# Kernel tuning notes

Hardware: AMD Instinct MI355X
Metric: run time of the kernel (lower is better)

## Reference

```python
import jax, jax.numpy as jnp
import numpy as np

B_COEF = 0.1          # position-offset scale 'b'
STRIDE = (1, 1)
PADDING = (1, 1)


def setup_inputs() -> dict:
    key = jax.random.key(0)
    k1, k2, k3 = jax.random.split(key, 3)
    x = jax.random.normal(k1, (16, 64, 128, 128), dtype=jnp.float32)
    kernel = jax.random.normal(k2, (128, 64, 3, 3), dtype=jnp.float32)
    bias = jax.random.normal(k3, (128,), dtype=jnp.float32)
    return {"x": x, "kernel": kernel, "bias": bias}


def _conv(inp, w):
    pads = [(PADDING[0], PADDING[0]), (PADDING[1], PADDING[1])]
    return jax.lax.conv_general_dilated(
        inp, w, window_strides=STRIDE, padding=pads,
        dimension_numbers=("NCHW", "OIHW", "NCHW"))


def reference(x, kernel, bias):
    # out[b,o,p] = sum_i x_unf[b,i,p] * (kernel_flat[o,i] + b*grid[p]) + bias[o]
    # = conv(x, kernel) + b*grid[p] * sum_i x_unf[b,i,p] + bias  (rank-1 separable)
    kh, kw = kernel.shape[2], kernel.shape[3]
    main = _conv(x, kernel)                                  # (B, O, Ho, Wo)
    H_out, W_out = main.shape[2], main.shape[3]

    # sum over in_channels and kernel window = ones-conv of channel-summed input
    ones_k = jnp.ones((1, 1, kh, kw), dtype=x.dtype)
    patch_sum = _conv(x.sum(axis=1, keepdims=True), ones_k)  # (B, 1, Ho, Wo)

    # Replicate torch meshgrid(arange(W_out), arange(H_out), indexing='ij')
    # -> flatten (W,H) row-major -> consumed as (H,W) row-major by the view.
    gx = jnp.arange(W_out)[:, None] + jnp.arange(H_out)[None, :]  # (Wo, Ho)
    grid2d = gx.reshape(-1).reshape(H_out, W_out).astype(x.dtype)  # (Ho, Wo)

    return main + B_COEF * grid2d * patch_sum + bias[None, :, None, None]
```

## Files before the change

### kernel.cpp

```cpp
#include <hip/hip_runtime.h>
#include <hip/hip_bf16.h>


typedef __attribute__((ext_vector_type(8))) short short8;
typedef __attribute__((ext_vector_type(4))) float f32x4;

#define B_COEF 0.1f
constexpr int CI = 64, CO = 128, H = 128, W = 128;
constexpr int XPAD = 72;

static __device__ inline short bf16s(float v) {
    __hip_bfloat16 b = __float2bfloat16(v);
    return *reinterpret_cast<short*>(&b);
}


__global__ __launch_bounds__(256)
void prep_x(const float* __restrict__ x, __hip_bfloat16* __restrict__ xt,
            float* __restrict__ S) {
    __shared__ float tile[64 * 132];
    __shared__ float psum[8 * 128];
    const int bx = blockIdx.x, b = blockIdx.y, tid = threadIdx.x;
    const int h = ((bx & 7) << 4) | (bx >> 3);
    const int q = tid & 31, cbase = tid >> 5;

    const float* xp = x + (((size_t)b * CI + cbase * 8) * H + h) * W + q * 4;
    f32x4 v[8];
#pragma unroll
    for (int it = 0; it < 8; ++it)
        v[it] = *(const f32x4*)(xp + (size_t)it * H * W);

    const int cw = 4 * (q ^ cbase);
    f32x4 sacc = v[0];
#pragma unroll
    for (int it = 0; it < 8; ++it) {
        *(f32x4*)&tile[(cbase * 8 + it) * 132 + cw] = v[it];
        if (it) sacc += v[it];
    }
    *(f32x4*)&psum[cbase * 128 + 4 * q] = sacc;
    __syncthreads();

    if (tid < 128) {
        float s = 0.0f;
#pragma unroll
        for (int g = 0; g < 8; ++g) s += psum[g * 128 + tid];
        S[((size_t)b * H + h) * W + tid] = s;
    }

    const int c8 = (tid & 7) * 8, wl = tid >> 3, sw = 4 * (tid & 7);
#pragma unroll
    for (int it = 0; it < 4; ++it) {
        int ww = wl + it * 32;
        short8 pk;
#pragma unroll
        for (int j = 0; j < 8; ++j)
            pk[j] = bf16s(tile[(c8 + j) * 132 + (ww ^ sw)]);
        *(short8*)(xt + (((size_t)b * H + h) * W + ww) * CI + c8) = pk;
    }
}

__global__ void prep_wq(const float* __restrict__ wgt, __hip_bfloat16* __restrict__ wq) {
    int idx = blockIdx.x * 256 + threadIdx.x;
    if (idx < 9 * CO * CI) {
        int tap = idx >> 13;
        int rem = idx & 8191;
        int oc = rem >> 6, ci = rem & 63;
        int kc = ci >> 5, j = ci & 31;
        wq[(((tap * 2 + kc) * CO + oc) << 5) + j] =
            __float2bfloat16(wgt[(oc * CI + ci) * 9 + tap]);
    }
}

__global__ __launch_bounds__(256, 2)
void conv_main(const __hip_bfloat16* __restrict__ xt,
               const __hip_bfloat16* __restrict__ wq,
               const float* __restrict__ S,
               const float* __restrict__ bias,
               float* __restrict__ out) {
    __shared__ __hip_bfloat16 xrow[4][130 * XPAD];
    __shared__ float ssum[2][132];

    const int tid = threadIdx.x, bx = blockIdx.x, b = blockIdx.y;
    const int strip = ((bx & 7) << 3) | (bx >> 3);
    const int h0 = strip * 2;
    const int lane = tid & 63, waveid = tid >> 6;
    const int lo16 = lane & 15, quad = lane >> 4;
    const int m0 = (waveid & 1) * 64, n0 = (waveid >> 1) * 64;

    const int c8 = (tid & 7) * 8, wl = tid >> 3;
#pragma unroll
    for (int r = 0; r < 4; ++r) {
        const int gh = h0 - 1 + r;
#pragma unroll
        for (int it = 0; it < 5; ++it) {
            int w = wl + it * 32;
            if (w < 130) {
                int gw = w - 1;
                short8 v = {0, 0, 0, 0, 0, 0, 0, 0};
                if (gh >= 0 && gh < H && gw >= 0 && gw < W)
                    v = *(const short8*)(xt + (((size_t)b * H + gh) * W + gw) * CI + c8);
                *(short8*)&xrow[r][w * XPAD + c8] = v;
            }
        }
    }
    if (tid < 130) {
        int gw = tid - 1;
        float s4[4] = {0.0f, 0.0f, 0.0f, 0.0f};
        if (gw >= 0 && gw < W) {
#pragma unroll
            for (int r = 0; r < 4; ++r) {
                int gh = h0 - 1 + r;
                if (gh >= 0 && gh < H) s4[r] = S[((size_t)b * H + gh) * W + gw];
            }
        }
        ssum[0][tid] = s4[0] + s4[1] + s4[2];
        ssum[1][tid] = s4[1] + s4[2] + s4[3];
    }
    __syncthreads();

    f32x4 acc[2][4][4] = {};

#pragma unroll
    for (int kh = 0; kh < 3; ++kh) {
#pragma unroll
        for (int kw = 0; kw < 3; ++kw) {
            const int tap = kh * 3 + kw;
            short8 bq[2][4];
#pragma unroll
            for (int kc = 0; kc < 2; ++kc)
#pragma unroll
                for (int ni = 0; ni < 4; ++ni)
                    bq[kc][ni] = *(const short8*)(
                        wq + (((tap * 2 + kc) * CO + n0 + ni * 16 + lo16) << 5) + quad * 8);
#pragma unroll
            for (int r = 0; r < 2; ++r) {
#pragma unroll
                for (int kc = 0; kc < 2; ++kc) {
                    short8 af[4];
#pragma unroll
                    for (int mi = 0; mi < 4; ++mi)
                        af[mi] = *(const short8*)
                            &xrow[kh + r][(m0 + mi * 16 + lo16 + kw) * XPAD + kc * 32 + quad * 8];
#pragma unroll
                    for (int mi = 0; mi < 4; ++mi)
#pragma unroll
                        for (int ni = 0; ni < 4; ++ni)
                            acc[r][mi][ni] = __builtin_amdgcn_mfma_f32_16x16x32_bf16(
                                af[mi], bq[kc][ni], acc[r][mi][ni], 0, 0, 0);
                }
            }
        }
    }

#pragma unroll
    for (int r = 0; r < 2; ++r) {
        const int h = h0 + r;
#pragma unroll
        for (int mi = 0; mi < 4; ++mi) {
            const int wbase = m0 + mi * 16 + quad * 4;
            float cs[6];
#pragma unroll
            for (int t = 0; t < 6; ++t) cs[t] = ssum[r][wbase + t];
            float ps[4], cf[4];
#pragma unroll
            for (int t = 0; t < 4; ++t) {
                ps[t] = cs[t] + cs[t + 1] + cs[t + 2];
                cf[t] = B_COEF * (float)(h + wbase + t);
            }
#pragma unroll
            for (int ni = 0; ni < 4; ++ni) {
                const int oc = n0 + ni * 16 + lo16;
                const float bv = bias[oc];
                f32x4 vv = acc[r][mi][ni];
#pragma unroll
                for (int t = 0; t < 4; ++t) vv[t] = vv[t] + cf[t] * ps[t] + bv;
                *(f32x4*)(out + (((size_t)b * CO + oc) * H + h) * W + wbase) = vv;
            }
        }
    }
}


constexpr int WPAD = 72;

__global__ void prep_w_fb(const float* __restrict__ wgt, __hip_bfloat16* __restrict__ wt) {
    int idx = blockIdx.x * 256 + threadIdx.x;
    if (idx < 9 * CO * CI) {
        int tap = idx / (CO * CI);
        int rem = idx - tap * (CO * CI);
        int oc = rem >> 6, ci = rem & 63;
        wt[idx] = __float2bfloat16(wgt[(oc * CI + ci) * 9 + tap]);
    }
}

__global__ __launch_bounds__(256, 2)
void conv_fb(const float* __restrict__ x, const __hip_bfloat16* __restrict__ wt,
             const float* __restrict__ bias, float* __restrict__ out) {
    __shared__ __hip_bfloat16 xrow[130 * XPAD];
    __shared__ __hip_bfloat16 wlds[CO * WPAD];
    __shared__ float colsum[132];

    const int tid = threadIdx.x;
    const int h = blockIdx.x, b = blockIdx.y;
    const int lane = tid & 63, waveid = tid >> 6;
    const int lo16 = lane & 15, quad = lane >> 4;
    const int m0 = (waveid & 1) * 64, n0 = (waveid >> 1) * 64;

    f32x4 acc[4][4] = {};
    if (tid < 132) colsum[tid] = 0.0f;
    const float* xb = x + (size_t)b * CI * H * W;

    const int w16 = tid & 15, cipl = (tid >> 4) & 3, rest0 = tid >> 6;

    for (int kh = 0; kh < 3; ++kh) {
        const int gh = h - 1 + kh;
        __syncthreads();
        for (int it = 0; it < 18; ++it) {
            int rest = rest0 + it * 4;
            int whi = rest % 9, ciph = rest / 9;
            int w = whi * 16 + w16;
            int ci0 = (ciph * 4 + cipl) * 2;
            int gw = w - 1;
            float x0 = 0.0f, x1 = 0.0f;
            if (w < 130 && gw >= 0 && gw < W && gh >= 0 && gh < H) {
                const float* p = xb + (size_t)ci0 * (H * W) + gh * W + gw;
                x0 = p[0];
                x1 = p[H * W];
            }
            if (w < 130) {
                __hip_bfloat162 pk;
                pk.x = __float2bfloat16(x0);
                pk.y = __float2bfloat16(x1);
                *(__hip_bfloat162*)&xrow[w * XPAD + ci0] = pk;
            }
            float cs = x0 + x1;
            cs += __shfl_xor(cs, 16);
            cs += __shfl_xor(cs, 32);
            if (quad == 0 && w < 130) atomicAdd(&colsum[w], cs);
        }
        for (int kw = 0; kw < 3; ++kw) {
            __syncthreads();
            {
                const __hip_bfloat16* wtap = wt + (kh * 3 + kw) * (CO * CI);
#pragma unroll
                for (int it = 0; it < 4; ++it) {
                    int j = tid + it * 256;
                    int oc = j >> 3, ch = (j & 7) * 8;
                    short8 v = *(const short8*)(wtap + oc * CI + ch);
                    *(short8*)&wlds[oc * WPAD + ch] = v;
                }
            }
            __syncthreads();
#pragma unroll
            for (int kc = 0; kc < 2; ++kc) {
                const int krow = kc * 32 + quad * 8;
                short8 af[4], bf[4];
#pragma unroll
                for (int mi = 0; mi < 4; ++mi)
                    af[mi] = *(const short8*)&xrow[(m0 + mi * 16 + lo16 + kw) * XPAD + krow];
#pragma unroll
                for (int ni = 0; ni < 4; ++ni)
                    bf[ni] = *(const short8*)&wlds[(n0 + ni * 16 + lo16) * WPAD + krow];
#pragma unroll
                for (int mi = 0; mi < 4; ++mi)
#pragma unroll
                    for (int ni = 0; ni < 4; ++ni)
                        acc[mi][ni] = __builtin_amdgcn_mfma_f32_16x16x32_bf16(
                            af[mi], bf[ni], acc[mi][ni], 0, 0, 0);
            }
        }
    }
    __syncthreads();
#pragma unroll
    for (int mi = 0; mi < 4; ++mi) {
        const int wbase = m0 + mi * 16 + quad * 4;
        float cs[6];
#pragma unroll
        for (int r = 0; r < 6; ++r) cs[r] = colsum[wbase + r];
        float ps[4], cf[4];
#pragma unroll
        for (int r = 0; r < 4; ++r) {
            ps[r] = cs[r] + cs[r + 1] + cs[r + 2];
            cf[r] = B_COEF * (float)(h + wbase + r);
        }
#pragma unroll
        for (int ni = 0; ni < 4; ++ni) {
            const int oc = n0 + ni * 16 + lo16;
            const float bv = bias[oc];
            f32x4 v = acc[mi][ni];
#pragma unroll
            for (int r = 0; r < 4; ++r) v[r] = v[r] + cf[r] * ps[r] + bv;
            *(f32x4*)(out + (((size_t)b * CO + oc) * H + h) * W + wbase) = v;
        }
    }
}


extern "C" void kernel_launch(void* const* d_in, const int* in_sizes, int n_in,
                              void* d_out, int out_size, void* d_ws, size_t ws_size,
                              hipStream_t stream) {
    const float* x    = (const float*)d_in[0];
    const float* wgt  = (const float*)d_in[1];
    const float* bias = (const float*)d_in[2];
    float* out = (float*)d_out;

    const size_t XT_BYTES = (size_t)16 * H * W * CI * 2;
    const size_t S_BYTES  = (size_t)16 * H * W * 4;
    const size_t WQ_BYTES = (size_t)9 * 2 * CO * 32 * 2;

    if (ws_size >= XT_BYTES + S_BYTES + WQ_BYTES) {
        __hip_bfloat16* xt = (__hip_bfloat16*)d_ws;
        float* S           = (float*)((char*)d_ws + XT_BYTES);
        __hip_bfloat16* wq = (__hip_bfloat16*)((char*)d_ws + XT_BYTES + S_BYTES);
        prep_x<<<dim3(H, 16), dim3(256), 0, stream>>>(x, xt, S);
        prep_wq<<<dim3(288), dim3(256), 0, stream>>>(wgt, wq);
        conv_main<<<dim3(H / 2, 16), dim3(256), 0, stream>>>(xt, wq, S, bias, out);
    } else {
        __hip_bfloat16* wt = (__hip_bfloat16*)d_ws;
        prep_w_fb<<<dim3(288), dim3(256), 0, stream>>>(wgt, wt);
        conv_fb<<<dim3(H, 16), dim3(256), 0, stream>>>(x, wt, bias, out);
    }
}
```

Baseline: 257.9 us.

## Shrink conv tile to one row by half-width for higher occupancy

Each conv_main block now computes one output row and half its width (64 pixels) instead of two full rows. Each wave covers all 64 pixels for 32 output channels. Accumulators drop from 32 to 8 MFMA tiles and shared memory shrinks, which lets launch bounds ask for 4 blocks per SIMD and gives a grid four times larger for better occupancy and balance. In exchange, the halo overlap per pixel is higher and weights are reloaded per block more often, so input-row reuse falls.

```diff
diff --git a/kernel.cpp b/kernel.cpp
--- a/kernel.cpp
+++ b/kernel.cpp
@@ -71,31 +71,31 @@
     }
 }
 
-__global__ __launch_bounds__(256, 2)
+__global__ __launch_bounds__(256, 4)
 void conv_main(const __hip_bfloat16* __restrict__ xt,
                const __hip_bfloat16* __restrict__ wq,
                const float* __restrict__ S,
                const float* __restrict__ bias,
                float* __restrict__ out) {
-    __shared__ __hip_bfloat16 xrow[4][130 * XPAD];
-    __shared__ float ssum[2][132];
+    __shared__ __hip_bfloat16 xrow[3][66 * XPAD];
+    __shared__ float ssum[68];
 
     const int tid = threadIdx.x, bx = blockIdx.x, b = blockIdx.y;
-    const int strip = ((bx & 7) << 3) | (bx >> 3);
-    const int h0 = strip * 2;
+    const int u = ((bx & 7) << 5) | (bx >> 3);
+    const int h = u >> 1, w0 = (u & 1) * 64;
     const int lane = tid & 63, waveid = tid >> 6;
     const int lo16 = lane & 15, quad = lane >> 4;
-    const int m0 = (waveid & 1) * 64, n0 = (waveid >> 1) * 64;
+    const int n0 = waveid * 32;
 
     const int c8 = (tid & 7) * 8, wl = tid >> 3;
 #pragma unroll
-    for (int r = 0; r < 4; ++r) {
-        const int gh = h0 - 1 + r;
-#pragma unroll
-        for (int it = 0; it < 5; ++it) {
+    for (int r = 0; r < 3; ++r) {
+        const int gh = h - 1 + r;
+#pragma unroll
+        for (int it = 0; it < 3; ++it) {
             int w = wl + it * 32;
-            if (w < 130) {
-                int gw = w - 1;
+            if (w < 66) {
+                int gw = w0 + w - 1;
                 short8 v = {0, 0, 0, 0, 0, 0, 0, 0};
                 if (gh >= 0 && gh < H && gw >= 0 && gw < W)
                     v = *(const short8*)(xt + (((size_t)b * H + gh) * W + gw) * CI + c8);
@@ -103,79 +103,71 @@
             }
         }
     }
-    if (tid < 130) {
-        int gw = tid - 1;
-        float s4[4] = {0.0f, 0.0f, 0.0f, 0.0f};
+    if (tid < 66) {
+        int gw = w0 + tid - 1;
+        float s = 0.0f;
         if (gw >= 0 && gw < W) {
 #pragma unroll
-            for (int r = 0; r < 4; ++r) {
-                int gh = h0 - 1 + r;
-                if (gh >= 0 && gh < H) s4[r] = S[((size_t)b * H + gh) * W + gw];
-            }
-        }
-        ssum[0][tid] = s4[0] + s4[1] + s4[2];
-        ssum[1][tid] = s4[1] + s4[2] + s4[3];
+            for (int r = 0; r < 3; ++r) {
+                int gh = h - 1 + r;
+                if (gh >= 0 && gh < H) s += S[((size_t)b * H + gh) * W + gw];
+            }
+        }
+        ssum[tid] = s;
     }
     __syncthreads();
 
-    f32x4 acc[2][4][4] = {};
+    f32x4 acc[4][2] = {};
 
 #pragma unroll
     for (int kh = 0; kh < 3; ++kh) {
 #pragma unroll
         for (int kw = 0; kw < 3; ++kw) {
             const int tap = kh * 3 + kw;
-            short8 bq[2][4];
+            short8 bq[2][2];
 #pragma unroll
             for (int kc = 0; kc < 2; ++kc)
 #pragma unroll
-                for (int ni = 0; ni < 4; ++ni)
+                for (int ni = 0; ni < 2; ++ni)
                     bq[kc][ni] = *(const short8*)(
                         wq + (((tap * 2 + kc) * CO + n0 + ni * 16 + lo16) << 5) + quad * 8);
 #pragma unroll
-            for (int r = 0; r < 2; ++r) {
-#pragma unroll
-                for (int kc = 0; kc < 2; ++kc) {
-                    short8 af[4];
-#pragma unroll
-                    for (int mi = 0; mi < 4; ++mi)
-                        af[mi] = *(const short8*)
-                            &xrow[kh + r][(m0 + mi * 16 + lo16 + kw) * XPAD + kc * 32 + quad * 8];
-#pragma unroll
-                    for (int mi = 0; mi < 4; ++mi)
-#pragma unroll
-                        for (int ni = 0; ni < 4; ++ni)
-                            acc[r][mi][ni] = __builtin_amdgcn_mfma_f32_16x16x32_bf16(
-                                af[mi], bq[kc][ni], acc[r][mi][ni], 0, 0, 0);
-                }
-            }
-        }
-    }
-
-#pragma unroll
-    for (int r = 0; r < 2; ++r) {
-        const int h = h0 + r;
-#pragma unroll
-        for (int mi = 0; mi < 4; ++mi) {
-            const int wbase = m0 + mi * 16 + quad * 4;
-            float cs[6];
-#pragma unroll
-            for (int t = 0; t < 6; ++t) cs[t] = ssum[r][wbase + t];
-            float ps[4], cf[4];
-#pragma unroll
-            for (int t = 0; t < 4; ++t) {
-                ps[t] = cs[t] + cs[t + 1] + cs[t + 2];
-                cf[t] = B_COEF * (float)(h + wbase + t);
-            }
-#pragma unroll
-            for (int ni = 0; ni < 4; ++ni) {
-                const int oc = n0 + ni * 16 + lo16;
-                const float bv = bias[oc];
-                f32x4 vv = acc[r][mi][ni];
-#pragma unroll
-                for (int t = 0; t < 4; ++t) vv[t] = vv[t] + cf[t] * ps[t] + bv;
-                *(f32x4*)(out + (((size_t)b * CO + oc) * H + h) * W + wbase) = vv;
-            }
+            for (int kc = 0; kc < 2; ++kc) {
+                short8 af[4];
+#pragma unroll
+                for (int mi = 0; mi < 4; ++mi)
+                    af[mi] = *(const short8*)
+                        &xrow[kh][(mi * 16 + lo16 + kw) * XPAD + kc * 32 + quad * 8];
+#pragma unroll
+                for (int mi = 0; mi < 4; ++mi)
+#pragma unroll
+                    for (int ni = 0; ni < 2; ++ni)
+                        acc[mi][ni] = __builtin_amdgcn_mfma_f32_16x16x32_bf16(
+                            af[mi], bq[kc][ni], acc[mi][ni], 0, 0, 0);
+            }
+        }
+    }
+
+#pragma unroll
+    for (int mi = 0; mi < 4; ++mi) {
+        const int wbase = mi * 16 + quad * 4;
+        float cs[6];
+#pragma unroll
+        for (int t = 0; t < 6; ++t) cs[t] = ssum[wbase + t];
+        float ps[4], cf[4];
+#pragma unroll
+        for (int t = 0; t < 4; ++t) {
+            ps[t] = cs[t] + cs[t + 1] + cs[t + 2];
+            cf[t] = B_COEF * (float)(h + w0 + wbase + t);
+        }
+#pragma unroll
+        for (int ni = 0; ni < 2; ++ni) {
+            const int oc = n0 + ni * 16 + lo16;
+            const float bv = bias[oc];
+            f32x4 v = acc[mi][ni];
+#pragma unroll
+            for (int t = 0; t < 4; ++t) v[t] = v[t] + cf[t] * ps[t] + bv;
+            *(f32x4*)(out + (((size_t)b * CO + oc) * H + h) * W + w0 + wbase) = v;
         }
     }
 }
@@ -314,7 +306,7 @@
         __hip_bfloat16* wq = (__hip_bfloat16*)((char*)d_ws + XT_BYTES + S_BYTES);
         prep_x<<<dim3(H, 16), dim3(256), 0, stream>>>(x, xt, S);
         prep_wq<<<dim3(288), dim3(256), 0, stream>>>(wgt, wq);
-        conv_main<<<dim3(H / 2, 16), dim3(256), 0, stream>>>(xt, wq, S, bias, out);
+        conv_main<<<dim3(2 * H, 16), dim3(256), 0, stream>>>(xt, wq, S, bias, out);
     } else {
         __hip_bfloat16* wt = (__hip_bfloat16*)d_ws;
         prep_w_fb<<<dim3(288), dim3(256), 0, stream>>>(wgt, wt);
```

Measured after the change: 238.9 us. 1.08x faster.
